# Optimization experiments

Hardware: AMD Instinct MI355X
Metric: run time of the kernel (lower is better)

## Reference

```python
import jax, jax.numpy as jnp
import numpy as np

N = 1_000_000        # points
V = 200_000          # occupied voxels
B = 4                # scans per batch
NUM_CLASSES = 20
DIM_POINT = 4
EPS = 1e-5


def bn(x, g, b):
    # eval-mode BatchNorm1d with running_mean=0, running_var=1
    return x * (g / jnp.sqrt(1.0 + EPS)) + b


def _lin(key, fi, fo):
    # kaiming-normal init, bias-free Linear stored as [in, out]
    return jax.random.normal(key, (fi, fo), jnp.float32) * np.sqrt(2.0 / fi)


def setup_inputs() -> dict:
    key = jax.random.key(0)
    ks = jax.random.split(key, 20)
    batch_ids = (jnp.arange(N) * B // N).astype(jnp.float32)[:, None]
    coords = jax.random.normal(ks[0], (N, DIM_POINT), jnp.float32)
    points = jnp.concatenate([batch_ids, coords], axis=1)           # [N, 1+dim_point]
    pv_ids = jax.random.randint(ks[1], (N,), 0, V, jnp.int64)       # point -> voxel
    ones, zeros = jnp.ones, jnp.zeros
    return {
        'points': points, 'point_voxel_ids': pv_ids,
        # point encoder: 4->32->64->32, each Linear(no bias)+BN+ReLU
        'pe_w1': _lin(ks[2], DIM_POINT, 32), 'pe_g1': ones(32), 'pe_b1': zeros(32),
        'pe_w2': _lin(ks[3], 32, 64),        'pe_g2': ones(64), 'pe_b2': zeros(64),
        'pe_w3': _lin(ks[4], 64, 32),        'pe_g3': ones(32), 'pe_b3': zeros(32),
        # voxel encoder (SparseUnet simplified to per-voxel 32->32->32)
        've_w1': _lin(ks[5], 32, 32), 've_g1': ones(32), 've_b1': zeros(32),
        've_w2': _lin(ks[6], 32, 32), 've_g2': ones(32), 've_b2': zeros(32),
        # fusion encoder: 64->64
        'fu_w': _lin(ks[7], 64, 64), 'fu_g': ones(64), 'fu_b': zeros(64),
        # FlattenSELayer: 64 -> 64//16 -> 64 with biases
        'se_w1': _lin(ks[8], 64, 4),  'se_b1': zeros(4),
        'se_w2': _lin(ks[9], 4, 64),  'se_b2': zeros(64),
        # main classifier 64->32->num_classes
        'cls_w1': _lin(ks[10], 64, 32), 'cls_g1': ones(32), 'cls_b1': zeros(32),
        'cls_w2': _lin(ks[11], 32, NUM_CLASSES),
        # aux classifier 32->32->num_classes
        'aux_w1': _lin(ks[12], 32, 32), 'aux_g1': ones(32), 'aux_b1': zeros(32),
        'aux_w2': _lin(ks[13], 32, NUM_CLASSES),
    }


def reference(points, point_voxel_ids,
              pe_w1, pe_g1, pe_b1, pe_w2, pe_g2, pe_b2, pe_w3, pe_g3, pe_b3,
              ve_w1, ve_g1, ve_b1, ve_w2, ve_g2, ve_b2,
              fu_w, fu_g, fu_b, se_w1, se_b1, se_w2, se_b2,
              cls_w1, cls_g1, cls_b1, cls_w2,
              aux_w1, aux_g1, aux_b1, aux_w2):
    batch_ids = points[:, 0].astype(jnp.int32)
    pv = point_voxel_ids.astype(jnp.int32)
    x = points[:, 1:]
    # point encoder
    pf = jax.nn.relu(bn(x @ pe_w1, pe_g1, pe_b1))
    pf = jax.nn.relu(bn(pf @ pe_w2, pe_g2, pe_b2))
    pf = jax.nn.relu(bn(pf @ pe_w3, pe_g3, pe_b3))               # [N,32]
    # voxel_max_pooling: point -> voxel scatter-max (empty voxels -> 0)
    vox = jax.ops.segment_max(pf, pv, num_segments=V)
    vox = jnp.where(jnp.isfinite(vox), vox, 0.0)                 # [V,32]
    # voxel encoder (SparseUnet stand-in); v1 is the aux feature tap
    v1 = jax.nn.relu(bn(vox @ ve_w1, ve_g1, ve_b1))              # [V,32]
    vf = jax.nn.relu(bn(v1 @ ve_w2, ve_g2, ve_b2))               # [V,32]
    # voxel_to_point gather + fusion
    pvf = vf[pv]                                                  # [N,32]
    fused = jnp.concatenate([pvf, pf], axis=1)                   # [N,64]
    fused = jax.nn.relu(bn(fused @ fu_w, fu_g, fu_b))
    # FlattenSELayer: per-scan mean -> gate -> residual scale
    sums = jax.ops.segment_sum(fused, batch_ids, num_segments=B)
    cnts = jax.ops.segment_sum(jnp.ones((fused.shape[0], 1), fused.dtype), batch_ids, num_segments=B)
    mean = sums / jnp.maximum(cnts, 1.0)                         # [B,64]
    gate = jax.nn.sigmoid(jax.nn.relu(mean @ se_w1 + se_b1) @ se_w2 + se_b2)
    fused = fused + fused * gate[batch_ids]
    # heads (dropout is identity at inference)
    out = jax.nn.relu(bn(fused @ cls_w1, cls_g1, cls_b1)) @ cls_w2      # [N,C]
    aux_out = jax.nn.relu(bn(v1 @ aux_w1, aux_g1, aux_b1)) @ aux_w2     # [V,C]
    return out, aux_out
```

## Files before the change

### kernel.cpp

```cpp
#include <hip/hip_runtime.h>
#include <hip/hip_bf16.h>

#define NPTS 1000000
#define NVOX 200000
#define NCLS 20

typedef __hip_bfloat16 bf16;
typedef __attribute__((ext_vector_type(8))) short bf16x8_t;
typedef __attribute__((ext_vector_type(4))) float f32x4_t;
#define MFMA16(a, b, c) __builtin_amdgcn_mfma_f32_16x16x32_bf16(a, b, c, 0, 0, 0)

constexpr size_t L_PTSC = 0;
constexpr size_t L_PV   = L_PTSC + (size_t)NPTS * 4;
constexpr size_t L_BID  = L_PV + NPTS;
constexpr size_t L_CNT  = L_BID + NPTS;
constexpr size_t L_BSUM = L_CNT + NVOX;
constexpr size_t L_BCNT = L_BSUM + 2048;
constexpr size_t L_GATE = L_BCNT + 4;
constexpr size_t L_FLAG = L_GATE + 256;
constexpr size_t L_OFFS = L_FLAG + 4;
constexpr size_t L_OFFW = L_OFFS + NVOX;
constexpr size_t L_BS1  = L_OFFW + NVOX;
constexpr size_t L_BB   = L_BS1 + 256;
constexpr size_t L_IDX  = L_BB + 256;
constexpr size_t L_W    = L_IDX + NPTS;
constexpr int O_PE1W = 0;      constexpr int O_PE1B = 128;
constexpr int O_PE2W = 160;    constexpr int O_PE2B = 2208;
constexpr int O_PE3W = 2272;   constexpr int O_PE3B = 4320;
constexpr int O_VE1W = 4352;   constexpr int O_VE1B = 5376;
constexpr int O_VE2W = 5408;   constexpr int O_VE2B = 6432;
constexpr int O_FUW  = 6464;   constexpr int O_FUB  = 10560;
constexpr int O_SE1W = 10624;  constexpr int O_SE1B = 10880;
constexpr int O_SE2W = 10884;  constexpr int O_SE2B = 11140;
constexpr int O_CLS1W = 11204; constexpr int O_CLS1B = 13252;
constexpr int O_CLS2W = 13284;
constexpr int O_AUX1W = 13924; constexpr int O_AUX1B = 14948;
constexpr int O_AUX2W = 14980;
constexpr int W_TOTAL = 15620;
constexpr size_t L_WT  = L_W + W_TOTAL;
static_assert((L_WT * 4) % 16 == 0, "WT alignment");
constexpr int WT_FU = 0;
constexpr int WT_C1 = 4096;
constexpr int WT_C2 = 6144;
constexpr int WT_2H = 7168;
constexpr int WT_2L = 9216;
constexpr int WT_3H = 11264;
constexpr int WT_3L = 13312;
constexpr int WT_U16 = 15360;
constexpr size_t L_VFU = L_WT + WT_U16 / 2;
constexpr size_t L_PFQ = L_VFU + (size_t)NVOX * 16;
constexpr size_t L_PFS = L_PFQ + (size_t)NPTS * 16;
static_assert((L_VFU * 4) % 16 == 0, "vf alignment");
static_assert((L_PFQ * 4) % 16 == 0, "pf alignment");
static_assert((L_PFS * 4) % 16 == 0, "pfs alignment");

static __device__ __forceinline__ float b2f(bf16 v) { return __bfloat162float(v); }
static __device__ __forceinline__ float us2f(unsigned short u) { return __uint_as_float((unsigned)u << 16); }
static __device__ __forceinline__ unsigned short f2us(float f) {
    unsigned u = __float_as_uint(f);
    u += 0x7fffu + ((u >> 16) & 1u);
    return (unsigned short)(u >> 16);
}
static __device__ __forceinline__ unsigned pack2(float a, float b) {
    return (unsigned)f2us(a) | ((unsigned)f2us(b) << 16);
}
static __device__ __forceinline__ void unpack2(unsigned u, float& a, float& b) {
    a = __uint_as_float(u << 16);
    b = __uint_as_float(u & 0xffff0000u);
}
static __device__ __forceinline__ float rdf(const void* p, size_t idx, int fp32) {
    return fp32 ? ((const float*)p)[idx] : b2f(((const bf16*)p)[idx]);
}
static __device__ __forceinline__ int detect_fp32(const void* pts_raw) {
    const unsigned short* ptsu = (const unsigned short*)pts_raw;
    return (ptsu[1] == 0 && ptsu[11] == 0) ? 1 : 0;
}
static __device__ __forceinline__ int detect_i64(const void* pv_raw) {
    const unsigned* pvu = (const unsigned*)pv_raw;
    return (pvu[1] == 0 && pvu[3] == 0 && pvu[5] == 0 && pvu[7] == 0) ? 1 : 0;
}

template <int K, int M, bool RELU, bool BIAS>
static __device__ __forceinline__ void dense(const float* __restrict__ x, float* __restrict__ y,
                                             const float* __restrict__ w, const float* __restrict__ b) {
#pragma unroll
    for (int j = 0; j < M; ++j) {
        float a = BIAS ? b[j] : 0.f;
#pragma unroll
        for (int k = 0; k < K; ++k) a = fmaf(x[k], w[k * M + j], a);
        y[j] = RELU ? fmaxf(a, 0.f) : a;
    }
}

static __device__ __forceinline__ int block_excl_scan(int v, int t) {
    __shared__ int sh[2][256];
    int cur = 0;
    sh[0][t] = v; __syncthreads();
#pragma unroll
    for (int off = 1; off < 256; off <<= 1) {
        int val = sh[cur][t];
        if (t >= off) val += sh[cur][t - off];
        sh[cur ^ 1][t] = val; __syncthreads();
        cur ^= 1;
    }
    return sh[cur][t] - v;
}

__global__ __launch_bounds__(256) void k0_norm(const void* __restrict__ pts_raw,
                                               const void* __restrict__ pv_raw,
                                               float4* __restrict__ ptsC,
                                               int* __restrict__ pvN,
                                               int* __restrict__ bidN,
                                               int* __restrict__ cnt,
                                               float* __restrict__ bcnt,
                                               int* __restrict__ rank) {
    int i = blockIdx.x * 256 + threadIdx.x;
    bool valid = i < NPTS;
    int fp32 = detect_fp32(pts_raw), i64 = detect_i64(pv_raw);
    int b = 0;
    if (valid) {
        float4 c;
        c.x = rdf(pts_raw, (size_t)i * 5 + 1, fp32);
        c.y = rdf(pts_raw, (size_t)i * 5 + 2, fp32);
        c.z = rdf(pts_raw, (size_t)i * 5 + 3, fp32);
        c.w = rdf(pts_raw, (size_t)i * 5 + 4, fp32);
        ptsC[i] = c;
        b = (int)rdf(pts_raw, (size_t)i * 5, fp32);
        bidN[i] = b;
        int v = i64 ? (int)((const long long*)pv_raw)[i] : ((const int*)pv_raw)[i];
        pvN[i] = v;
        rank[i] = atomicAdd(&cnt[v], 1);
    }
    __shared__ int sb0, sflag;
    if (threadIdx.x == 0) { sb0 = b; sflag = 1; }
    __syncthreads();
    if (valid && b != sb0) sflag = 0;
    __syncthreads();
    if (sflag) {
        if (threadIdx.x == 0) {
            int vc = NPTS - blockIdx.x * 256; if (vc > 256) vc = 256;
            atomicAdd(&bcnt[sb0], (float)vc);
        }
    } else if (valid) {
        atomicAdd(&bcnt[b], 1.f);
    }
}

struct WPtrs {
    const void *pe_w1, *pe_g1, *pe_b1, *pe_w2, *pe_g2, *pe_b2, *pe_w3, *pe_g3, *pe_b3;
    const void *ve_w1, *ve_g1, *ve_b1, *ve_w2, *ve_g2, *ve_b2;
    const void *fu_w, *fu_g, *fu_b;
    const void *se_w1, *se_b1, *se_w2, *se_b2;
    const void *cls_w1, *cls_g1, *cls_b1, *cls_w2;
    const void *aux_w1, *aux_g1, *aux_b1, *aux_w2;
};

static __device__ void foldw(float* d, const void* w, const void* g, int K, int M, int fp32) {
    const float INV = 0.9999950000374997f;
    for (int idx = threadIdx.x; idx < K * M; idx += 256)
        d[idx] = rdf(w, idx, fp32) * (rdf(g, idx % M, fp32) * INV);
}
static __device__ void cpv(float* d, const void* s, int n, int fp32) {
    for (int idx = threadIdx.x; idx < n; idx += 256) d[idx] = rdf(s, idx, fp32);
}

__global__ void k0_prep(WPtrs p, const void* __restrict__ pts_raw, float* __restrict__ W,
                        unsigned short* __restrict__ WT) {
    int f = detect_fp32(pts_raw);
    foldw(W + O_PE1W, p.pe_w1, p.pe_g1, 4, 32, f);   cpv(W + O_PE1B, p.pe_b1, 32, f);
    foldw(W + O_PE2W, p.pe_w2, p.pe_g2, 32, 64, f);  cpv(W + O_PE2B, p.pe_b2, 64, f);
    foldw(W + O_PE3W, p.pe_w3, p.pe_g3, 64, 32, f);  cpv(W + O_PE3B, p.pe_b3, 32, f);
    foldw(W + O_VE1W, p.ve_w1, p.ve_g1, 32, 32, f);  cpv(W + O_VE1B, p.ve_b1, 32, f);
    foldw(W + O_VE2W, p.ve_w2, p.ve_g2, 32, 32, f);  cpv(W + O_VE2B, p.ve_b2, 32, f);
    foldw(W + O_FUW,  p.fu_w,  p.fu_g,  64, 64, f);  cpv(W + O_FUB,  p.fu_b, 64, f);
    cpv(W + O_SE1W, p.se_w1, 256, f);  cpv(W + O_SE1B, p.se_b1, 4, f);
    cpv(W + O_SE2W, p.se_w2, 256, f);  cpv(W + O_SE2B, p.se_b2, 64, f);
    foldw(W + O_CLS1W, p.cls_w1, p.cls_g1, 64, 32, f); cpv(W + O_CLS1B, p.cls_b1, 32, f);
    cpv(W + O_CLS2W, p.cls_w2, 640, f);
    foldw(W + O_AUX1W, p.aux_w1, p.aux_g1, 32, 32, f); cpv(W + O_AUX1B, p.aux_b1, 32, f);
    cpv(W + O_AUX2W, p.aux_w2, 640, f);
    __syncthreads();
    unsigned short* wtfu = WT + WT_FU;
    unsigned short* wtc1 = WT + WT_C1;
    unsigned short* wtc2 = WT + WT_C2;
    unsigned short* wt2h = WT + WT_2H;
    unsigned short* wt2l = WT + WT_2L;
    unsigned short* wt3h = WT + WT_3H;
    unsigned short* wt3l = WT + WT_3L;
    for (int idx = threadIdx.x; idx < 4096; idx += 256) {
        int n = idx >> 6, k = idx & 63;
        wtfu[idx] = f2us(W[O_FUW + k * 64 + n]);
    }
    for (int idx = threadIdx.x; idx < 2048; idx += 256) {
        int n = idx >> 6, k = idx & 63;
        wtc1[idx] = f2us(W[O_CLS1W + k * 32 + n]);
    }
    for (int idx = threadIdx.x; idx < 1024; idx += 256) {
        int n = idx >> 5, k = idx & 31;
        wtc2[idx] = (n < NCLS) ? f2us(W[O_CLS2W + k * NCLS + n]) : (unsigned short)0;
    }
    for (int idx = threadIdx.x; idx < 2048; idx += 256) {
        int n = idx >> 5, k = idx & 31;
        float v = W[O_PE2W + k * 64 + n];
        unsigned short hi = f2us(v);
        wt2h[idx] = hi;
        wt2l[idx] = f2us(v - us2f(hi));
    }
    for (int idx = threadIdx.x; idx < 2048; idx += 256) {
        int n = idx >> 6, k = idx & 63;
        float v = W[O_PE3W + k * 32 + n];
        unsigned short hi = f2us(v);
        wt3h[idx] = hi;
        wt3l[idx] = f2us(v - us2f(hi));
    }
}

__global__ __launch_bounds__(256) void k_scan1(const int* __restrict__ cnt, int* __restrict__ bs) {
    int t = threadIdx.x;
    int base = blockIdx.x * 1024 + t * 4;
    int s = 0;
#pragma unroll
    for (int k = 0; k < 4; ++k) { int idx = base + k; if (idx < NVOX) s += cnt[idx]; }
    __shared__ int red[256];
    red[t] = s; __syncthreads();
    for (int off = 128; off > 0; off >>= 1) { if (t < off) red[t] += red[t + off]; __syncthreads(); }
    if (t == 0) bs[blockIdx.x] = red[0];
}

__global__ __launch_bounds__(256) void k_scan2(const int* __restrict__ bs, int* __restrict__ bb, int nb) {
    int t = threadIdx.x;
    int v = (t < nb) ? bs[t] : 0;
    int e = block_excl_scan(v, t);
    bb[t] = e;
}

__global__ __launch_bounds__(256) void k_scan3(const int* __restrict__ cnt, const int* __restrict__ bb,
                                               int* __restrict__ offs) {
    int t = threadIdx.x;
    int base = blockIdx.x * 1024 + t * 4;
    int c[4]; int s = 0;
#pragma unroll
    for (int k = 0; k < 4; ++k) { int idx = base + k; c[k] = (idx < NVOX) ? cnt[idx] : 0; s += c[k]; }
    int run = bb[blockIdx.x] + block_excl_scan(s, t);
#pragma unroll
    for (int k = 0; k < 4; ++k) {
        int idx = base + k;
        if (idx < NVOX) { offs[idx] = run; run += c[k]; }
    }
}

__global__ __launch_bounds__(256) void k1_mfma(const float4* __restrict__ ptsC,
                                               const float* __restrict__ W,
                                               const unsigned short* __restrict__ WT2H,
                                               const unsigned short* __restrict__ WT2L,
                                               const unsigned short* __restrict__ WT3H,
                                               const unsigned short* __restrict__ WT3L,
                                               const int* __restrict__ pv,
                                               const int* __restrict__ rank,
                                               const int* __restrict__ offs,
                                               uint4* __restrict__ pf_q,
                                               uint4* __restrict__ pf_s) {
    __shared__ __align__(16) unsigned short hth[4][16][72];
    __shared__ __align__(16) unsigned short htl[4][16][72];
    __shared__ __align__(16) unsigned short pt[4][16][40];
    int t = threadIdx.x;
    int lane = t & 63, w = t >> 6;
    int m = lane & 15, quad = lane >> 4;
    int i0 = blockIdx.x * 256;

    float w1[32], b1[8];
#pragma unroll
    for (int k = 0; k < 4; ++k)
#pragma unroll
        for (int j = 0; j < 8; ++j) w1[k * 8 + j] = W[O_PE1W + k * 32 + quad * 8 + j];
#pragma unroll
    for (int j = 0; j < 8; ++j) b1[j] = W[O_PE1B + quad * 8 + j];
    bf16x8_t b2h[4], b2l[4], b3h[2][2], b3l[2][2];
    float bias2[4], bias3[2];
#pragma unroll
    for (int tn = 0; tn < 4; ++tn) {
        b2h[tn] = *(const bf16x8_t*)(WT2H + (tn * 16 + m) * 32 + quad * 8);
        b2l[tn] = *(const bf16x8_t*)(WT2L + (tn * 16 + m) * 32 + quad * 8);
        bias2[tn] = W[O_PE2B + tn * 16 + m];
    }
#pragma unroll
    for (int tn = 0; tn < 2; ++tn) {
#pragma unroll
        for (int kh = 0; kh < 2; ++kh) {
            b3h[tn][kh] = *(const bf16x8_t*)(WT3H + (tn * 16 + m) * 64 + kh * 32 + quad * 8);
            b3l[tn][kh] = *(const bf16x8_t*)(WT3L + (tn * 16 + m) * 64 + kh * 32 + quad * 8);
        }
        bias3[tn] = W[O_PE3B + tn * 16 + m];
    }
    int nval = NPTS - i0; if (nval > 256) nval = 256;
    int ntiles = (nval - w * 64 >= 64) ? 4 : 0;

#pragma unroll 1
    for (int tt = 0; tt < ntiles; ++tt) {
        int rbase = i0 + w * 64 + tt * 16;
        int arow = rbase + m;
        float4 c = ptsC[arow];
        int sp = offs[pv[arow]] + rank[arow];
        union { unsigned u[4]; bf16x8_t v; } ah, al;
#pragma unroll
        for (int p = 0; p < 4; ++p) {
            unsigned hu = 0, lu = 0;
#pragma unroll
            for (int s = 0; s < 2; ++s) {
                int j = 2 * p + s;
                float h = b1[j];
                h = fmaf(c.x, w1[0 * 8 + j], h);
                h = fmaf(c.y, w1[1 * 8 + j], h);
                h = fmaf(c.z, w1[2 * 8 + j], h);
                h = fmaf(c.w, w1[3 * 8 + j], h);
                h = fmaxf(h, 0.f);
                unsigned short hi = f2us(h);
                unsigned short lo = f2us(h - us2f(hi));
                hu |= (unsigned)hi << (16 * s);
                lu |= (unsigned)lo << (16 * s);
            }
            ah.u[p] = hu; al.u[p] = lu;
        }
#pragma unroll
        for (int tn = 0; tn < 4; ++tn) {
            f32x4_t acc = {0.f, 0.f, 0.f, 0.f};
            acc = MFMA16(ah.v, b2h[tn], acc);
            acc = MFMA16(ah.v, b2l[tn], acc);
            acc = MFMA16(al.v, b2h[tn], acc);
#pragma unroll
            for (int e = 0; e < 4; ++e) {
                float v = fmaxf(acc[e] + bias2[tn], 0.f);
                unsigned short hi = f2us(v);
                hth[w][quad * 4 + e][tn * 16 + m] = hi;
                htl[w][quad * 4 + e][tn * 16 + m] = f2us(v - us2f(hi));
            }
        }
        bf16x8_t x0h = *(const bf16x8_t*)&hth[w][m][quad * 8];
        bf16x8_t x1h = *(const bf16x8_t*)&hth[w][m][32 + quad * 8];
        bf16x8_t x0l = *(const bf16x8_t*)&htl[w][m][quad * 8];
        bf16x8_t x1l = *(const bf16x8_t*)&htl[w][m][32 + quad * 8];
#pragma unroll
        for (int tn = 0; tn < 2; ++tn) {
            f32x4_t acc = {0.f, 0.f, 0.f, 0.f};
            acc = MFMA16(x0h, b3h[tn][0], acc);
            acc = MFMA16(x1h, b3h[tn][1], acc);
            acc = MFMA16(x0h, b3l[tn][0], acc);
            acc = MFMA16(x1h, b3l[tn][1], acc);
            acc = MFMA16(x0l, b3h[tn][0], acc);
            acc = MFMA16(x1l, b3h[tn][1], acc);
#pragma unroll
            for (int e = 0; e < 4; ++e)
                pt[w][quad * 4 + e][tn * 16 + m] = f2us(fmaxf(acc[e] + bias3[tn], 0.f));
        }
        uint4 q = *(const uint4*)&pt[w][m][quad * 8];
        pf_q[(size_t)arow * 4 + quad] = q;
        pf_s[(size_t)sp * 4 + quad] = q;
    }
}

__global__ __launch_bounds__(256) void k_voxmlp(const int* __restrict__ offs, const int* __restrict__ cnt,
                                                const uint4* __restrict__ pf_s,
                                                const float* __restrict__ W,
                                                const void* __restrict__ pts_raw,
                                                unsigned* __restrict__ vf_u,
                                                void* __restrict__ outbase) {
    int v = blockIdx.x * 256 + threadIdx.x;
    if (v >= NVOX) return;
    int of32 = detect_fp32(pts_raw);
    float mx[32];
#pragma unroll
    for (int c = 0; c < 32; ++c) mx[c] = 0.f;
    int s = offs[v], n = cnt[v];
    for (int p = 0; p < n; ++p) {
        size_t base = (size_t)(s + p) * 4;
#pragma unroll
        for (int t = 0; t < 4; ++t) {
            uint4 q = pf_s[base + t];
            float a, b;
            unpack2(q.x, a, b); mx[8*t+0] = fmaxf(mx[8*t+0], a); mx[8*t+1] = fmaxf(mx[8*t+1], b);
            unpack2(q.y, a, b); mx[8*t+2] = fmaxf(mx[8*t+2], a); mx[8*t+3] = fmaxf(mx[8*t+3], b);
            unpack2(q.z, a, b); mx[8*t+4] = fmaxf(mx[8*t+4], a); mx[8*t+5] = fmaxf(mx[8*t+5], b);
            unpack2(q.w, a, b); mx[8*t+6] = fmaxf(mx[8*t+6], a); mx[8*t+7] = fmaxf(mx[8*t+7], b);
        }
    }
    float v1[32], vf[32], a1[32], o[20];
    dense<32, 32, true, true>(mx, v1, W + O_VE1W, W + O_VE1B);
    dense<32, 32, true, true>(v1, vf, W + O_VE2W, W + O_VE2B);
#pragma unroll
    for (int c = 0; c < 16; ++c) vf_u[(size_t)v * 16 + c] = pack2(vf[2*c], vf[2*c+1]);
    dense<32, 32, true, true>(v1, a1, W + O_AUX1W, W + O_AUX1B);
    dense<32, 20, false, false>(a1, o, W + O_AUX2W, nullptr);
    if (of32) {
        float* auxf = (float*)outbase + (size_t)NPTS * NCLS + (size_t)v * NCLS;
#pragma unroll
        for (int t = 0; t < NCLS; ++t) auxf[t] = o[t];
    } else {
        unsigned* auxu = (unsigned*)((bf16*)outbase + (size_t)NPTS * NCLS);
#pragma unroll
        for (int t = 0; t < 10; ++t) auxu[(size_t)v * 10 + t] = pack2(o[2*t], o[2*t+1]);
    }
}

__global__ __launch_bounds__(256) void k3_mfma(const int* __restrict__ bid, const int* __restrict__ pv,
                                               const uint4* __restrict__ pf_q,
                                               const uint4* __restrict__ vf_q,
                                               const float* __restrict__ W,
                                               const unsigned short* __restrict__ WTfu,
                                               float* __restrict__ bsum8) {
    __shared__ int sbid[256];
    __shared__ float red[4][64];
    __shared__ int sflag;
    int t = threadIdx.x;
    int i0 = blockIdx.x * 256;
    int nval = NPTS - i0; if (nval > 256) nval = 256;
    if (t < nval) sbid[t] = bid[i0 + t];
    if (t == 0) sflag = (bid[i0] == bid[i0 + nval - 1]) ? 1 : 0;

    int lane = t & 63, w = t >> 6;
    int m = lane & 15, quad = lane >> 4;
    bf16x8_t bw0[4], bw1[4];
    float bias[4];
#pragma unroll
    for (int tn = 0; tn < 4; ++tn) {
        bw0[tn] = *(const bf16x8_t*)(WTfu + (tn * 16 + m) * 64 + quad * 8);
        bw1[tn] = *(const bf16x8_t*)(WTfu + (tn * 16 + m) * 64 + 32 + quad * 8);
        bias[tn] = W[O_FUB + tn * 16 + m];
    }
    __syncthreads();
    int uni = sflag;
    int b0 = sbid[0];
    int rep = (blockIdx.x & 7) * 256;
    int ntiles = (nval - w * 64 >= 64) ? 4 : 0;

    float csum[4] = {0.f, 0.f, 0.f, 0.f};
#pragma unroll
    for (int tt = 0; tt < 4; ++tt) {
        if (tt >= ntiles) break;
        int rbase = i0 + w * 64 + tt * 16;
        int arow = rbase + m;
        int pvr = pv[arow];
        uint4 va = vf_q[(size_t)pvr * 4 + quad];
        uint4 vb = pf_q[(size_t)arow * 4 + quad];
        bf16x8_t a0 = *(bf16x8_t*)&va;
        bf16x8_t a1 = *(bf16x8_t*)&vb;
        float f[4][4];
#pragma unroll
        for (int tn = 0; tn < 4; ++tn) {
            f32x4_t acc = {0.f, 0.f, 0.f, 0.f};
            acc = MFMA16(a0, bw0[tn], acc);
            acc = MFMA16(a1, bw1[tn], acc);
#pragma unroll
            for (int e = 0; e < 4; ++e) f[tn][e] = fmaxf(acc[e] + bias[tn], 0.f);
        }
        if (uni) {
#pragma unroll
            for (int tn = 0; tn < 4; ++tn) {
                float s = f[tn][0] + f[tn][1] + f[tn][2] + f[tn][3];
                s += __shfl_xor(s, 16);
                s += __shfl_xor(s, 32);
                csum[tn] += s;
            }
        } else {
#pragma unroll
            for (int tn = 0; tn < 4; ++tn)
#pragma unroll
                for (int e = 0; e < 4; ++e)
                    atomicAdd(&bsum8[rep + sbid[rbase - i0 + quad * 4 + e] * 64 + tn * 16 + m], f[tn][e]);
        }
    }
    if (uni) {
        float mine = quad == 0 ? csum[0] : quad == 1 ? csum[1] : quad == 2 ? csum[2] : csum[3];
        red[w][quad * 16 + m] = mine;
        __syncthreads();
        if (t < 64) {
            float s = red[0][t] + red[1][t] + red[2][t] + red[3][t];
            atomicAdd(&bsum8[rep + b0 * 64 + t], s);
        }
    }
}

__global__ void k4_gate(const float* __restrict__ bsum8, const float* __restrict__ bcnt,
                        const float* __restrict__ W, float* __restrict__ gate) {
    __shared__ float m[4][64];
    __shared__ float hid[4][4];
    int tid = threadIdx.x, b = tid >> 6, c = tid & 63;
    float s = 0.f;
#pragma unroll
    for (int r = 0; r < 8; ++r) s += bsum8[r * 256 + tid];
    m[b][c] = s / fmaxf(bcnt[b], 1.f);
    __syncthreads();
    if (c < 4) {
        const float* w = W + O_SE1W;
        float a = (W + O_SE1B)[c];
        for (int k = 0; k < 64; ++k) a = fmaf(m[b][k], w[k * 4 + c], a);
        hid[b][c] = fmaxf(a, 0.f);
    }
    __syncthreads();
    const float* w2 = W + O_SE2W;
    float g = (W + O_SE2B)[c];
#pragma unroll
    for (int h = 0; h < 4; ++h) g = fmaf(hid[b][h], w2[h * 64 + c], g);
    gate[tid] = 1.f + 1.f / (1.f + expf(-g));
}

__global__ __launch_bounds__(256) void k5_mfma(const int* __restrict__ bid, const int* __restrict__ pv,
                                               const uint4* __restrict__ pf_q,
                                               const uint4* __restrict__ vf_q,
                                               const float* __restrict__ W,
                                               const unsigned short* __restrict__ WTfu,
                                               const unsigned short* __restrict__ WTc1,
                                               const unsigned short* __restrict__ WTc2,
                                               const float* __restrict__ gate,
                                               const void* __restrict__ pts_raw,
                                               void* __restrict__ out) {
    __shared__ float sg[256];
    __shared__ int sbid[256];
    __shared__ int sflag;
    __shared__ __align__(16) unsigned short ft[4][16][72];
    __shared__ __align__(16) unsigned short ht[4][16][40];
    __shared__ float ot[4][16][20];
    int t = threadIdx.x;
    int i0 = blockIdx.x * 256;
    int nval = NPTS - i0; if (nval > 256) nval = 256;
    sg[t] = gate[t];
    if (t < nval) sbid[t] = bid[i0 + t];
    if (t == 0) sflag = (bid[i0] == bid[i0 + nval - 1]) ? 1 : 0;

    int lane = t & 63, w = t >> 6;
    int m = lane & 15, quad = lane >> 4;
    bf16x8_t bfu0[4], bfu1[4], bc10[2], bc11[2], bc2[2];
    float biasfu[4], biasc1[2];
#pragma unroll
    for (int tn = 0; tn < 4; ++tn) {
        bfu0[tn] = *(const bf16x8_t*)(WTfu + (tn * 16 + m) * 64 + quad * 8);
        bfu1[tn] = *(const bf16x8_t*)(WTfu + (tn * 16 + m) * 64 + 32 + quad * 8);
        biasfu[tn] = W[O_FUB + tn * 16 + m];
    }
#pragma unroll
    for (int tn = 0; tn < 2; ++tn) {
        bc10[tn] = *(const bf16x8_t*)(WTc1 + (tn * 16 + m) * 64 + quad * 8);
        bc11[tn] = *(const bf16x8_t*)(WTc1 + (tn * 16 + m) * 64 + 32 + quad * 8);
        bc2[tn]  = *(const bf16x8_t*)(WTc2 + (tn * 16 + m) * 32 + quad * 8);
        biasc1[tn] = W[O_CLS1B + tn * 16 + m];
    }
    __syncthreads();
    int uni = sflag;
    int of32 = detect_fp32(pts_raw);
    int ntiles = (nval - w * 64 >= 64) ? 4 : 0;

#pragma unroll 1
    for (int tt = 0; tt < ntiles; ++tt) {
        int rbase = i0 + w * 64 + tt * 16;
        int arow = rbase + m;
        int pvr = pv[arow];
        uint4 va = vf_q[(size_t)pvr * 4 + quad];
        uint4 vb = pf_q[(size_t)arow * 4 + quad];
        bf16x8_t a0 = *(bf16x8_t*)&va;
        bf16x8_t a1 = *(bf16x8_t*)&vb;
        float gcol[4];
        if (uni) {
#pragma unroll
            for (int tn = 0; tn < 4; ++tn) gcol[tn] = sg[sbid[0] * 64 + tn * 16 + m];
        }
#pragma unroll
        for (int tn = 0; tn < 4; ++tn) {
            f32x4_t acc = {0.f, 0.f, 0.f, 0.f};
            acc = MFMA16(a0, bfu0[tn], acc);
            acc = MFMA16(a1, bfu1[tn], acc);
#pragma unroll
            for (int e = 0; e < 4; ++e) {
                float fv = fmaxf(acc[e] + biasfu[tn], 0.f);
                float g = uni ? gcol[tn] : sg[sbid[rbase - i0 + quad * 4 + e] * 64 + tn * 16 + m];
                ft[w][quad * 4 + e][tn * 16 + m] = f2us(fv * g);
            }
        }
        bf16x8_t c0 = *(const bf16x8_t*)&ft[w][m][quad * 8];
        bf16x8_t c1 = *(const bf16x8_t*)&ft[w][m][32 + quad * 8];
#pragma unroll
        for (int tn = 0; tn < 2; ++tn) {
            f32x4_t acc = {0.f, 0.f, 0.f, 0.f};
            acc = MFMA16(c0, bc10[tn], acc);
            acc = MFMA16(c1, bc11[tn], acc);
#pragma unroll
            for (int e = 0; e < 4; ++e)
                ht[w][quad * 4 + e][tn * 16 + m] = f2us(fmaxf(acc[e] + biasc1[tn], 0.f));
        }
        bf16x8_t d0 = *(const bf16x8_t*)&ht[w][m][quad * 8];
#pragma unroll
        for (int tn = 0; tn < 2; ++tn) {
            f32x4_t acc = {0.f, 0.f, 0.f, 0.f};
            acc = MFMA16(d0, bc2[tn], acc);
            int c = tn * 16 + m;
            if (c < NCLS) {
#pragma unroll
                for (int e = 0; e < 4; ++e) ot[w][quad * 4 + e][c] = acc[e];
            }
        }
        if (of32) {
            float* of = (float*)out + (size_t)rbase * NCLS;
#pragma unroll
            for (int k = 0; k < 5; ++k) {
                int idx = k * 64 + lane;
                of[idx] = ((const float*)ot[w])[idx];
            }
        } else {
            unsigned* ow = (unsigned*)((unsigned short*)out + (size_t)rbase * NCLS);
#pragma unroll
            for (int k = 0; k < 3; ++k) {
                int idx = k * 64 + lane;
                if (idx < 160) {
                    int p = idx / 10, c2 = idx - p * 10;
                    ow[idx] = pack2(ot[w][p][2 * c2], ot[w][p][2 * c2 + 1]);
                }
            }
        }
    }
}

extern "C" void kernel_launch(void* const* d_in, const int* in_sizes, int n_in,
                              void* d_out, int out_size, void* d_ws, size_t ws_size,
                              hipStream_t stream) {
    WPtrs p;
    p.pe_w1 = d_in[2];  p.pe_g1 = d_in[3];  p.pe_b1 = d_in[4];
    p.pe_w2 = d_in[5];  p.pe_g2 = d_in[6];  p.pe_b2 = d_in[7];
    p.pe_w3 = d_in[8];  p.pe_g3 = d_in[9];  p.pe_b3 = d_in[10];
    p.ve_w1 = d_in[11]; p.ve_g1 = d_in[12]; p.ve_b1 = d_in[13];
    p.ve_w2 = d_in[14]; p.ve_g2 = d_in[15]; p.ve_b2 = d_in[16];
    p.fu_w  = d_in[17]; p.fu_g  = d_in[18]; p.fu_b  = d_in[19];
    p.se_w1 = d_in[20]; p.se_b1 = d_in[21];
    p.se_w2 = d_in[22]; p.se_b2 = d_in[23];
    p.cls_w1 = d_in[24]; p.cls_g1 = d_in[25]; p.cls_b1 = d_in[26];
    p.cls_w2 = d_in[27];
    p.aux_w1 = d_in[28]; p.aux_g1 = d_in[29]; p.aux_b1 = d_in[30];
    p.aux_w2 = d_in[31];

    float* base = (float*)d_ws;
    float4* ptsC = (float4*)(base + L_PTSC);
    int*   pvN  = (int*)(base + L_PV);
    int*   bidN = (int*)(base + L_BID);
    int*   cnt  = (int*)(base + L_CNT);
    float* bsum8 = base + L_BSUM;
    float* bcnt = base + L_BCNT;
    float* gate = base + L_GATE;
    int*   offs = (int*)(base + L_OFFS);
    int*   bs1  = (int*)(base + L_BS1);
    int*   bb   = (int*)(base + L_BB);
    int*   rank = (int*)(base + L_IDX);
    float* W    = base + L_W;
    unsigned short* WT = (unsigned short*)(base + L_WT);
    unsigned short* wtfu = WT + WT_FU;
    unsigned short* wtc1 = WT + WT_C1;
    unsigned short* wtc2 = WT + WT_C2;
    unsigned short* wt2h = WT + WT_2H;
    unsigned short* wt2l = WT + WT_2L;
    unsigned short* wt3h = WT + WT_3H;
    unsigned short* wt3l = WT + WT_3L;
    unsigned* vf_u = (unsigned*)(base + L_VFU);
    uint4* pf_q = (uint4*)(base + L_PFQ);
    uint4* pf_s = (uint4*)(base + L_PFS);

    constexpr int NBP = (NPTS + 255) / 256;
    constexpr int NBV = (NVOX + 255) / 256;
    constexpr int NBS = (NVOX + 1023) / 1024;
    constexpr int NBM = (NPTS + 255) / 256;

    hipMemsetAsync(cnt, 0, (NVOX + 2048 + 4) * sizeof(float), stream);
    k0_norm<<<NBP, 256, 0, stream>>>(d_in[0], d_in[1], ptsC, pvN, bidN, cnt, bcnt, rank);
    k0_prep<<<1, 256, 0, stream>>>(p, d_in[0], W, WT);
    k_scan1<<<NBS, 256, 0, stream>>>(cnt, bs1);
    k_scan2<<<1, 256, 0, stream>>>(bs1, bb, NBS);
    k_scan3<<<NBS, 256, 0, stream>>>(cnt, bb, offs);
    k1_mfma<<<NBM, 256, 0, stream>>>(ptsC, W, wt2h, wt2l, wt3h, wt3l, pvN, rank, offs, pf_q, pf_s);
    k_voxmlp<<<NBV, 256, 0, stream>>>(offs, cnt, pf_s, W, d_in[0], vf_u, d_out);
    k3_mfma<<<NBM, 256, 0, stream>>>(bidN, pvN, pf_q, (const uint4*)vf_u, W, wtfu, bsum8);
    k4_gate<<<1, 256, 0, stream>>>(bsum8, bcnt, W, gate);
    k5_mfma<<<NBM, 256, 0, stream>>>(bidN, pvN, pf_q, (const uint4*)vf_u, W, wtfu, wtc1, wtc2, gate, d_in[0], d_out);
}
```

Before: 560.2 us.

## Fuse input normalization and voxel counting into point-encoder kernel, add scatter pass

Merges the k0_norm pass (reading raw points, batch ids, voxel ids, atomic counting and rank assignment) into the point-encoder MFMA kernel, which now reads raw points directly instead of a normalized float4 copy. Since the voxel offsets are not known until after the scan, the scatter of point features into voxel-sorted order moves to a new k_scat kernel that copies pf_q into pf_s. This drops the ptsC intermediate buffer and one full read/write pass over the points. In exchange it adds a separate gather/scatter kernel that re-reads the 64MB-scale pf_q, and strided raw-point reads inside the MFMA kernel.

```diff
diff --git a/kernel.cpp b/kernel.cpp
--- a/kernel.cpp
+++ b/kernel.cpp
@@ -106,46 +106,6 @@
     return sh[cur][t] - v;
 }
 
-__global__ __launch_bounds__(256) void k0_norm(const void* __restrict__ pts_raw,
-                                               const void* __restrict__ pv_raw,
-                                               float4* __restrict__ ptsC,
-                                               int* __restrict__ pvN,
-                                               int* __restrict__ bidN,
-                                               int* __restrict__ cnt,
-                                               float* __restrict__ bcnt,
-                                               int* __restrict__ rank) {
-    int i = blockIdx.x * 256 + threadIdx.x;
-    bool valid = i < NPTS;
-    int fp32 = detect_fp32(pts_raw), i64 = detect_i64(pv_raw);
-    int b = 0;
-    if (valid) {
-        float4 c;
-        c.x = rdf(pts_raw, (size_t)i * 5 + 1, fp32);
-        c.y = rdf(pts_raw, (size_t)i * 5 + 2, fp32);
-        c.z = rdf(pts_raw, (size_t)i * 5 + 3, fp32);
-        c.w = rdf(pts_raw, (size_t)i * 5 + 4, fp32);
-        ptsC[i] = c;
-        b = (int)rdf(pts_raw, (size_t)i * 5, fp32);
-        bidN[i] = b;
-        int v = i64 ? (int)((const long long*)pv_raw)[i] : ((const int*)pv_raw)[i];
-        pvN[i] = v;
-        rank[i] = atomicAdd(&cnt[v], 1);
-    }
-    __shared__ int sb0, sflag;
-    if (threadIdx.x == 0) { sb0 = b; sflag = 1; }
-    __syncthreads();
-    if (valid && b != sb0) sflag = 0;
-    __syncthreads();
-    if (sflag) {
-        if (threadIdx.x == 0) {
-            int vc = NPTS - blockIdx.x * 256; if (vc > 256) vc = 256;
-            atomicAdd(&bcnt[sb0], (float)vc);
-        }
-    } else if (valid) {
-        atomicAdd(&bcnt[b], 1.f);
-    }
-}
-
 struct WPtrs {
     const void *pe_w1, *pe_g1, *pe_b1, *pe_w2, *pe_g2, *pe_b2, *pe_w3, *pe_g3, *pe_b3;
     const void *ve_w1, *ve_g1, *ve_b1, *ve_w2, *ve_g2, *ve_b2;
@@ -249,17 +209,19 @@
     }
 }
 
-__global__ __launch_bounds__(256) void k1_mfma(const float4* __restrict__ ptsC,
-                                               const float* __restrict__ W,
-                                               const unsigned short* __restrict__ WT2H,
-                                               const unsigned short* __restrict__ WT2L,
-                                               const unsigned short* __restrict__ WT3H,
-                                               const unsigned short* __restrict__ WT3L,
-                                               const int* __restrict__ pv,
-                                               const int* __restrict__ rank,
-                                               const int* __restrict__ offs,
-                                               uint4* __restrict__ pf_q,
-                                               uint4* __restrict__ pf_s) {
+__global__ __launch_bounds__(256) void k1_fused(const void* __restrict__ pts_raw,
+                                                const void* __restrict__ pv_raw,
+                                                const float* __restrict__ W,
+                                                const unsigned short* __restrict__ WT2H,
+                                                const unsigned short* __restrict__ WT2L,
+                                                const unsigned short* __restrict__ WT3H,
+                                                const unsigned short* __restrict__ WT3L,
+                                                int* __restrict__ pvN,
+                                                int* __restrict__ bidN,
+                                                int* __restrict__ cnt,
+                                                float* __restrict__ bcnt,
+                                                int* __restrict__ rank,
+                                                uint4* __restrict__ pf_q) {
     __shared__ __align__(16) unsigned short hth[4][16][72];
     __shared__ __align__(16) unsigned short htl[4][16][72];
     __shared__ __align__(16) unsigned short pt[4][16][40];
@@ -267,6 +229,7 @@
     int lane = t & 63, w = t >> 6;
     int m = lane & 15, quad = lane >> 4;
     int i0 = blockIdx.x * 256;
+    int fp32 = detect_fp32(pts_raw), i64 = detect_i64(pv_raw);
 
     float w1[32], b1[8];
 #pragma unroll
@@ -299,8 +262,11 @@
     for (int tt = 0; tt < ntiles; ++tt) {
         int rbase = i0 + w * 64 + tt * 16;
         int arow = rbase + m;
-        float4 c = ptsC[arow];
-        int sp = offs[pv[arow]] + rank[arow];
+        float4 c;
+        c.x = rdf(pts_raw, (size_t)arow * 5 + 1, fp32);
+        c.y = rdf(pts_raw, (size_t)arow * 5 + 2, fp32);
+        c.z = rdf(pts_raw, (size_t)arow * 5 + 3, fp32);
+        c.w = rdf(pts_raw, (size_t)arow * 5 + 4, fp32);
         union { unsigned u[4]; bf16x8_t v; } ah, al;
 #pragma unroll
         for (int p = 0; p < 4; ++p) {
@@ -354,8 +320,41 @@
         }
         uint4 q = *(const uint4*)&pt[w][m][quad * 8];
         pf_q[(size_t)arow * 4 + quad] = q;
-        pf_s[(size_t)sp * 4 + quad] = q;
-    }
+    }
+
+    int i = i0 + t;
+    bool valid = t < nval;
+    int b = 0, rk = 0;
+    if (valid) {
+        b = (int)rdf(pts_raw, (size_t)i * 5, fp32);
+        bidN[i] = b;
+        int v = i64 ? (int)((const long long*)pv_raw)[i] : ((const int*)pv_raw)[i];
+        pvN[i] = v;
+        rk = atomicAdd(&cnt[v], 1);
+    }
+    __shared__ int sb0, sflag;
+    if (t == 0) { sb0 = b; sflag = 1; }
+    __syncthreads();
+    if (valid && b != sb0) sflag = 0;
+    __syncthreads();
+    if (sflag) {
+        if (t == 0) atomicAdd(&bcnt[sb0], (float)nval);
+    } else if (valid) {
+        atomicAdd(&bcnt[b], 1.f);
+    }
+    if (valid) rank[i] = rk;
+}
+
+__global__ __launch_bounds__(256) void k_scat(const int* __restrict__ pv,
+                                              const int* __restrict__ rank,
+                                              const int* __restrict__ offs,
+                                              const uint4* __restrict__ pf_q,
+                                              uint4* __restrict__ pf_s) {
+    int tid = blockIdx.x * 256 + threadIdx.x;
+    int i = tid >> 2, quad = tid & 3;
+    if (i >= NPTS) return;
+    int sp = offs[pv[i]] + rank[i];
+    pf_s[(size_t)sp * 4 + quad] = pf_q[(size_t)i * 4 + quad];
 }
 
 __global__ __launch_bounds__(256) void k_voxmlp(const int* __restrict__ offs, const int* __restrict__ cnt,
@@ -635,7 +634,6 @@
     p.aux_w2 = d_in[31];
 
     float* base = (float*)d_ws;
-    float4* ptsC = (float4*)(base + L_PTSC);
     int*   pvN  = (int*)(base + L_PV);
     int*   bidN = (int*)(base + L_BID);
     int*   cnt  = (int*)(base + L_CNT);
@@ -659,18 +657,19 @@
     uint4* pf_q = (uint4*)(base + L_PFQ);
     uint4* pf_s = (uint4*)(base + L_PFS);
 
-    constexpr int NBP = (NPTS + 255) / 256;
     constexpr int NBV = (NVOX + 255) / 256;
     constexpr int NBS = (NVOX + 1023) / 1024;
     constexpr int NBM = (NPTS + 255) / 256;
+    constexpr int NBSC = (NPTS * 4 + 255) / 256;
 
     hipMemsetAsync(cnt, 0, (NVOX + 2048 + 4) * sizeof(float), stream);
-    k0_norm<<<NBP, 256, 0, stream>>>(d_in[0], d_in[1], ptsC, pvN, bidN, cnt, bcnt, rank);
     k0_prep<<<1, 256, 0, stream>>>(p, d_in[0], W, WT);
+    k1_fused<<<NBM, 256, 0, stream>>>(d_in[0], d_in[1], W, wt2h, wt2l, wt3h, wt3l,
+                                      pvN, bidN, cnt, bcnt, rank, pf_q);
     k_scan1<<<NBS, 256, 0, stream>>>(cnt, bs1);
     k_scan2<<<1, 256, 0, stream>>>(bs1, bb, NBS);
     k_scan3<<<NBS, 256, 0, stream>>>(cnt, bb, offs);
-    k1_mfma<<<NBM, 256, 0, stream>>>(ptsC, W, wt2h, wt2l, wt3h, wt3l, pvN, rank, offs, pf_q, pf_s);
+    k_scat<<<NBSC, 256, 0, stream>>>(pvN, rank, offs, pf_q, pf_s);
     k_voxmlp<<<NBV, 256, 0, stream>>>(offs, cnt, pf_s, W, d_in[0], vf_u, d_out);
     k3_mfma<<<NBM, 256, 0, stream>>>(bidN, pvN, pf_q, (const uint4*)vf_u, W, wtfu, bsum8);
     k4_gate<<<1, 256, 0, stream>>>(bsum8, bcnt, W, gate);
```

New measurement: 554.2 us. About the same (-1.1%).
